# Kernel optimization log

Measured on AMD Instinct MI355X. Metric: run time of the kernel, lower is better.

## Reference

```python
import jax, jax.numpy as jnp
import numpy as np

N_NODES = 50000
HIDDEN = 128
N_EDGES = 800000


def gcn_conv(x, edge_index, W, b):
    # PyG GCNConv: h = x @ W (no bias); add self-loops; symmetric norm; scatter-add; + bias
    h = x @ W  # [N, H]
    row, col = edge_index[0], edge_index[1]
    sl = jnp.arange(N_NODES)
    row_f = jnp.concatenate([row, sl])
    col_f = jnp.concatenate([col, sl])
    ones = jnp.ones(row_f.shape[0], dtype=x.dtype)
    deg = jax.ops.segment_sum(ones, col_f, num_segments=N_NODES)  # in-degree incl self-loop
    dinv = jnp.where(deg > 0, jax.lax.rsqrt(deg), 0.0)
    norm = dinv[row_f] * dinv[col_f]  # [E+N]
    msgs = h[row_f] * norm[:, None]   # gather + scale
    out = jax.ops.segment_sum(msgs, col_f, num_segments=N_NODES)  # scatter-add
    return out + b


def setup_inputs() -> dict:
    key = jax.random.key(0)
    ks = jax.random.split(key, 12)
    H = HIDDEN
    s = 1.0 / np.sqrt(H)
    x = jax.random.normal(ks[0], (N_NODES, H), dtype=jnp.float32)
    edge_index = jax.random.randint(ks[1], (2, N_EDGES), 0, N_NODES, dtype=jnp.int64)
    W1 = jax.random.uniform(ks[2], (H, H), jnp.float32, -s, s)
    b1 = jax.random.uniform(ks[3], (H,), jnp.float32, -s, s)
    W2 = jax.random.uniform(ks[4], (H, H), jnp.float32, -s, s)
    b2 = jax.random.uniform(ks[5], (H,), jnp.float32, -s, s)
    s2 = 1.0 / np.sqrt(2 * H)
    We1 = jax.random.uniform(ks[6], (2 * H, H), jnp.float32, -s2, s2)
    be1 = jax.random.uniform(ks[7], (H,), jnp.float32, -s2, s2)
    We2 = jax.random.uniform(ks[8], (H, 1), jnp.float32, -s, s)
    be2 = jax.random.uniform(ks[9], (1,), jnp.float32, -s, s)
    return {"x": x, "edge_index": edge_index, "W1": W1, "b1": b1, "W2": W2,
            "b2": b2, "We1": We1, "be1": be1, "We2": We2, "be2": be2}


def reference(x, edge_index, W1, b1, W2, b2, We1, be1, We2, be2):
    h = jax.nn.relu(gcn_conv(x, edge_index, W1, b1))
    h = jax.nn.relu(gcn_conv(h, edge_index, W2, b2))
    row, col = edge_index[0], edge_index[1]
    ef = jnp.concatenate([h[row], h[col]], axis=1)  # [E, 2H]
    z = jax.nn.relu(ef @ We1 + be1)
    p = jax.nn.sigmoid(z @ We2 + be2)  # [E, 1]
    return p.squeeze(-1)
```

## Files before the change

### kernel.cpp

```cpp
#include <hip/hip_runtime.h>
#include <math.h>

#define NND 50000
#define HD  128
#define NE  800000
#define NBK 196
#define BINB 391
#define NCH 391

typedef unsigned short u16;
typedef unsigned int   u32;
typedef __attribute__((ext_vector_type(8))) short bf16x8;
typedef __attribute__((ext_vector_type(4))) float f32x4;

__device__ __forceinline__ float bf2f(u32 u) {
  union { u32 i; float f; } v; v.i = u << 16; return v.f;
}
__device__ __forceinline__ u16 f2bf(float f) {
  union { float f; u32 i; } v; v.f = f;
  return (u16)((v.i + 0x7FFFu + ((v.i >> 16) & 1u)) >> 16);
}
__device__ __forceinline__ float4 unpack4(uint2 m) {
  float4 r;
  r.x = bf2f(m.x & 0xFFFFu); r.y = bf2f(m.x >> 16);
  r.z = bf2f(m.y & 0xFFFFu); r.w = bf2f(m.y >> 16);
  return r;
}

__global__ __launch_bounds__(256) void k_hist(const int* __restrict__ col, u32* __restrict__ bhist) {
  __shared__ u32 lh[NBK];
  int tid = threadIdx.x;
  if (tid < NBK) lh[tid] = 0;
  __syncthreads();
  int e0 = blockIdx.x * 2048;
  #pragma unroll
  for (int s = 0; s < 8; ++s) {
    int e = e0 + s * 256 + tid;
    if (e < NE) atomicAdd(&lh[col[e] >> 8], 1u);
  }
  __syncthreads();
  if (tid < NBK && lh[tid]) atomicAdd(&bhist[tid], lh[tid]);
}

__global__ __launch_bounds__(256) void k_bscan(const u32* __restrict__ bhist, u32* __restrict__ bbase,
                                               u32* __restrict__ bcur) {
  __shared__ u32 ws[4];
  int tid = threadIdx.x, lane = tid & 63, wid = tid >> 6;
  u32 d = (tid < NBK) ? bhist[tid] : 0;
  u32 x = d;
  #pragma unroll
  for (int off = 1; off < 64; off <<= 1) {
    u32 y = __shfl_up(x, off);
    if (lane >= off) x += y;
  }
  if (lane == 63) ws[wid] = x;
  __syncthreads();
  u32 woff = 0;
  for (int w = 0; w < wid; ++w) woff += ws[w];
  if (tid < NBK) { bbase[tid] = woff + x - d; bcur[tid] = woff + x - d; }
}

__global__ __launch_bounds__(256) void k_bin(const int* __restrict__ row, const int* __restrict__ col,
                                             u32* __restrict__ bcur, uint2* __restrict__ recs) {
  __shared__ u32 lcount[NBK], lbase[NBK];
  int tid = threadIdx.x;
  if (tid < NBK) lcount[tid] = 0;
  __syncthreads();
  int e0 = blockIdx.x * 2048;
  u32 rank[8]; int cv[8];
  #pragma unroll
  for (int s = 0; s < 8; ++s) {
    int e = e0 + s * 256 + tid;
    if (e < NE) {
      cv[s] = col[e];
      rank[s] = atomicAdd(&lcount[cv[s] >> 8], 1u);
    }
  }
  __syncthreads();
  if (tid < NBK && lcount[tid]) lbase[tid] = atomicAdd(&bcur[tid], lcount[tid]);
  __syncthreads();
  #pragma unroll
  for (int s = 0; s < 8; ++s) {
    int e = e0 + s * 256 + tid;
    if (e < NE) {
      int c = cv[s];
      u32 slot = lbase[c >> 8] + rank[s];
      recs[slot] = make_uint2((u32)row[e] | (((u32)c & 255u) << 16), (u32)e);
    }
  }
}

__global__ __launch_bounds__(256) void k_fine(const u32* __restrict__ bhist, const u32* __restrict__ bbase,
                                              const uint2* __restrict__ recs, uint2* __restrict__ sre,
                                              int* __restrict__ ptr, float* __restrict__ dinv) {
  __shared__ u32 lh[256];
  __shared__ u32 ws[4];
  int b = blockIdx.x, tid = threadIdx.x, lane = tid & 63, wid = tid >> 6;
  u32 base = bbase[b], cnt = bhist[b];
  lh[tid] = 0;
  __syncthreads();
  for (u32 i = tid; i < cnt; i += 256) atomicAdd(&lh[(recs[base + i].x >> 16) & 255u], 1u);
  __syncthreads();
  u32 ci = lh[tid];
  u32 x = ci;
  #pragma unroll
  for (int off = 1; off < 64; off <<= 1) {
    u32 y = __shfl_up(x, off);
    if (lane >= off) x += y;
  }
  if (lane == 63) ws[wid] = x;
  __syncthreads();
  u32 woff = 0;
  for (int w = 0; w < wid; ++w) woff += ws[w];
  u32 excl = woff + x - ci;
  int node = b * 256 + tid;
  if (node <= NND) ptr[node] = (int)(base + excl);
  if (node < NND) dinv[node] = rsqrtf((float)(ci + 1));
  __syncthreads();
  lh[tid] = excl;
  __syncthreads();
  for (u32 i = tid; i < cnt; i += 256) {
    uint2 rec = recs[base + i];
    u32 r = atomicAdd(&lh[(rec.x >> 16) & 255u], 1u);
    sre[base + r] = make_uint2(rec.x & 0xFFFFu, rec.y);
  }
}

__global__ __launch_bounds__(256) void k_wprep(const float* __restrict__ W1, const float* __restrict__ W2,
                                               const float* __restrict__ We1,
                                               u16* __restrict__ t1h, u16* __restrict__ t1l,
                                               u16* __restrict__ t2h, u16* __restrict__ t2l,
                                               u16* __restrict__ teh, u16* __restrict__ tel) {
  int idx = blockIdx.x * 256 + threadIdx.x;
  float w;
  u16 *dh, *dl;
  int j;
  if (idx < 16384) {
    j = idx; int n = j >> 7, k = j & 127;
    w = W1[k * 128 + n]; dh = t1h; dl = t1l;
  } else if (idx < 32768) {
    j = idx - 16384; int n = j >> 7, k = j & 127;
    w = W2[k * 128 + n]; dh = t2h; dl = t2l;
  } else {
    j = idx - 32768; int n = j >> 7, k = j & 127;
    w = (n < 128) ? We1[k * 128 + n] : We1[(128 + k) * 128 + (n - 128)];
    dh = teh; dl = tel;
  }
  int n = j >> 7, k = j & 127;
  int sidx = n * 128 + ((((k >> 3) ^ (n & 7))) << 3) + (k & 7);
  u16 hi = f2bf(w);
  float res = w - bf2f((u32)hi);
  dh[sidx] = hi;
  dl[sidx] = f2bf(res);
}

template<bool AFP32>
__global__ __launch_bounds__(512) void k_mm(const void* __restrict__ Xv,
                                            const u16* __restrict__ Whi, const u16* __restrict__ Wlo,
                                            u16* __restrict__ OUT, const float* __restrict__ scale,
                                            int ostride, int ooff) {
  __shared__ __align__(16) u16 Bh[128 * 128];
  __shared__ __align__(16) u16 Bl[128 * 128];
  int tid = threadIdx.x;
  {
    const uint4* gh = (const uint4*)Whi;
    const uint4* gl = (const uint4*)Wlo;
    uint4* lh = (uint4*)Bh;
    uint4* ll = (uint4*)Bl;
    #pragma unroll
    for (int i = 0; i < 4; ++i) {
      lh[tid + i * 512] = gh[tid + i * 512];
      ll[tid + i * 512] = gl[tid + i * 512];
    }
  }
  __syncthreads();
  int wid = tid >> 6, lane = tid & 63;
  int m16 = lane & 15, kg = lane >> 4;
  for (int chunk = blockIdx.x; chunk < NCH; chunk += gridDim.x) {
    int arow = chunk * 128 + wid * 16 + m16;
    int ar = (arow < NND) ? arow : NND - 1;
    bf16x8 afrag[4];
    if (AFP32) {
      const float* X = (const float*)Xv + (size_t)ar * 128 + kg * 8;
      #pragma unroll
      for (int ks = 0; ks < 4; ++ks) {
        float4 a = *(const float4*)(X + ks * 32);
        float4 b = *(const float4*)(X + ks * 32 + 4);
        union { u32 w[4]; bf16x8 v; } u;
        u.w[0] = (u32)f2bf(a.x) | ((u32)f2bf(a.y) << 16);
        u.w[1] = (u32)f2bf(a.z) | ((u32)f2bf(a.w) << 16);
        u.w[2] = (u32)f2bf(b.x) | ((u32)f2bf(b.y) << 16);
        u.w[3] = (u32)f2bf(b.z) | ((u32)f2bf(b.w) << 16);
        afrag[ks] = u.v;
      }
    } else {
      const u16* X = (const u16*)Xv + (size_t)ar * 128 + kg * 8;
      #pragma unroll
      for (int ks = 0; ks < 4; ++ks) afrag[ks] = *(const bf16x8*)(X + ks * 32);
    }
    int crow0 = chunk * 128 + wid * 16 + kg * 4;
    float sc[4];
    #pragma unroll
    for (int j = 0; j < 4; ++j)
      sc[j] = (scale != nullptr && crow0 + j < NND) ? scale[crow0 + j] : 1.0f;
    #pragma unroll
    for (int t = 0; t < 8; ++t) {
      int coln = t * 16 + m16;
      f32x4 acc = {0.f, 0.f, 0.f, 0.f};
      #pragma unroll
      for (int ks = 0; ks < 4; ++ks) {
        int c8 = (ks * 4 + kg) ^ (coln & 7);
        bf16x8 bhf = *(const bf16x8*)(Bh + coln * 128 + c8 * 8);
        bf16x8 blf = *(const bf16x8*)(Bl + coln * 128 + c8 * 8);
        acc = __builtin_amdgcn_mfma_f32_16x16x32_bf16(afrag[ks], bhf, acc, 0, 0, 0);
        acc = __builtin_amdgcn_mfma_f32_16x16x32_bf16(afrag[ks], blf, acc, 0, 0, 0);
      }
      #pragma unroll
      for (int j = 0; j < 4; ++j) {
        int r = crow0 + j;
        if (r < NND) OUT[(size_t)r * ostride + ooff + coln] = f2bf(acc[j] * sc[j]);
      }
    }
  }
}

__global__ __launch_bounds__(256) void k_gather(const int* __restrict__ ptr, const uint2* __restrict__ sre,
                                                const float* __restrict__ dinv, const u16* __restrict__ Ts,
                                                u16* __restrict__ H, const float* __restrict__ bias) {
  int wid = threadIdx.x >> 6, lane = threadIdx.x & 63;
  int q = lane & 31, eo = lane >> 5;
  int v = blockIdx.x * 4 + wid; if (v >= NND) return;
  int p0 = ptr[v], p1 = ptr[v + 1];
  const uint2* T2 = (const uint2*)Ts;
  float4 acc = make_float4(0.f, 0.f, 0.f, 0.f);
  if (eo == 0) acc = unpack4(T2[(size_t)v * 32 + q]);
  for (int j2 = p0; j2 < p1; j2 += 16) {
    bool ok[8]; int r[8];
    #pragma unroll
    for (int s = 0; s < 8; ++s) {
      int j = j2 + s * 2 + eo;
      ok[s] = j < p1;
      r[s] = (int)sre[ok[s] ? j : p0].x;
    }
    float4 m[8];
    #pragma unroll
    for (int s = 0; s < 8; ++s) m[s] = unpack4(T2[(size_t)r[s] * 32 + q]);
    #pragma unroll
    for (int s = 0; s < 8; ++s)
      if (ok[s]) { acc.x += m[s].x; acc.y += m[s].y; acc.z += m[s].z; acc.w += m[s].w; }
  }
  acc.x += __shfl_xor(acc.x, 32);
  acc.y += __shfl_xor(acc.y, 32);
  acc.z += __shfl_xor(acc.z, 32);
  acc.w += __shfl_xor(acc.w, 32);
  if (eo == 0) {
    float s = dinv[v];
    float4 b = ((const float4*)bias)[q];
    float o0 = fmaxf(fmaf(acc.x, s, b.x), 0.f);
    float o1 = fmaxf(fmaf(acc.y, s, b.y), 0.f);
    float o2 = fmaxf(fmaf(acc.z, s, b.z), 0.f);
    float o3 = fmaxf(fmaf(acc.w, s, b.w), 0.f);
    uint2 o;
    o.x = (u32)f2bf(o0) | ((u32)f2bf(o1) << 16);
    o.y = (u32)f2bf(o2) | ((u32)f2bf(o3) << 16);
    ((uint2*)H)[(size_t)v * 32 + q] = o;
  }
}

__global__ __launch_bounds__(256) void k_edge(const int* __restrict__ ptr, const uint2* __restrict__ sre,
                                              const u16* __restrict__ UV,
                                              const float* __restrict__ be1, const float* __restrict__ We2,
                                              const float* __restrict__ be2, float* __restrict__ out) {
  int wid = threadIdx.x >> 6, lane = threadIdx.x & 63;
  int q = lane & 31, eo = lane >> 5;
  int c = blockIdx.x * 4 + wid; if (c >= NND) return;
  int p0 = ptr[c], p1 = ptr[c + 1];
  if (p0 == p1) return;
  const uint2* UV2 = (const uint2*)UV;
  float4 vv = unpack4(UV2[(size_t)c * 64 + 32 + q]);
  float4 b = ((const float4*)be1)[q];
  vv.x += b.x; vv.y += b.y; vv.z += b.z; vv.w += b.w;
  float4 w2 = ((const float4*)We2)[q];
  float bias2 = be2[0];
  for (int j2 = p0; j2 < p1; j2 += 16) {
    bool ok[8]; uint2 e[8];
    #pragma unroll
    for (int s = 0; s < 8; ++s) {
      int j = j2 + s * 2 + eo;
      ok[s] = j < p1;
      e[s] = sre[ok[s] ? j : p0];
    }
    float4 u[8];
    #pragma unroll
    for (int s = 0; s < 8; ++s) u[s] = unpack4(UV2[(size_t)e[s].x * 64 + q]);
    float p[8];
    #pragma unroll
    for (int s = 0; s < 8; ++s) {
      p[s] = fmaxf(u[s].x + vv.x, 0.f) * w2.x
           + fmaxf(u[s].y + vv.y, 0.f) * w2.y
           + fmaxf(u[s].z + vv.z, 0.f) * w2.z
           + fmaxf(u[s].w + vv.w, 0.f) * w2.w;
    }
    #pragma unroll
    for (int off = 16; off; off >>= 1) {
      #pragma unroll
      for (int s = 0; s < 8; ++s) p[s] += __shfl_xor(p[s], off);
    }
    if (q == 0) {
      #pragma unroll
      for (int s = 0; s < 8; ++s)
        if (ok[s]) out[e[s].y] = 1.f / (1.f + __expf(-(p[s] + bias2)));
    }
  }
}

extern "C" void kernel_launch(void* const* d_in, const int* in_sizes, int n_in,
                              void* d_out, int out_size, void* d_ws, size_t ws_size,
                              hipStream_t stream) {
  const float* x   = (const float*)d_in[0];
  const int*   ei  = (const int*)d_in[1];
  const float* W1  = (const float*)d_in[2];
  const float* b1  = (const float*)d_in[3];
  const float* W2  = (const float*)d_in[4];
  const float* b2  = (const float*)d_in[5];
  const float* We1 = (const float*)d_in[6];
  const float* be1 = (const float*)d_in[7];
  const float* We2 = (const float*)d_in[8];
  const float* be2 = (const float*)d_in[9];
  float* out = (float*)d_out;

  const int* row  = ei;
  const int* colp = ei + NE;

  if (ws_size < (size_t)16166240 * 4) return;
  int*   ptr    = (int*)d_ws;
  float* dinv   = (float*)d_ws + 50064;
  u32*   bhist  = (u32*)d_ws + 100112;
  u32*   bbase  = (u32*)d_ws + 100308;
  u32*   bcur   = (u32*)d_ws + 100504;
  uint2* recs   = (uint2*)((u32*)d_ws + 100704);
  uint2* sre    = (uint2*)((u32*)d_ws + 1700704);
  u16*   t1h    = (u16*)((u32*)d_ws + 3300704);
  u16*   t1l    = (u16*)((u32*)d_ws + 3308896);
  u16*   t2h    = (u16*)((u32*)d_ws + 3317088);
  u16*   t2l    = (u16*)((u32*)d_ws + 3325280);
  u16*   teh    = (u16*)((u32*)d_ws + 3333472);
  u16*   tel    = (u16*)((u32*)d_ws + 3349856);
  u16*   Ts     = (u16*)((u32*)d_ws + 3366240);
  u16*   H      = (u16*)((u32*)d_ws + 6566240);
  u16*   UV     = (u16*)((u32*)d_ws + 9766240);

  hipMemsetAsync(bhist, 0, NBK * sizeof(u32), stream);
  k_wprep<<<256, 256, 0, stream>>>(W1, W2, We1, t1h, t1l, t2h, t2l, teh, tel);
  k_hist <<<BINB, 256, 0, stream>>>(colp, bhist);
  k_bscan<<<1, 256, 0, stream>>>(bhist, bbase, bcur);
  k_bin  <<<BINB, 256, 0, stream>>>(row, colp, bcur, recs);
  k_fine <<<NBK, 256, 0, stream>>>(bhist, bbase, recs, sre, ptr, dinv);

  int node_grid = (NND + 3) / 4;

  k_mm<true><<<196, 512, 0, stream>>>(x, t1h, t1l, Ts, dinv, 128, 0);
  k_gather<<<node_grid, 256, 0, stream>>>(ptr, sre, dinv, Ts, H, b1);

  k_mm<false><<<196, 512, 0, stream>>>(H, t2h, t2l, Ts, dinv, 128, 0);
  k_gather<<<node_grid, 256, 0, stream>>>(ptr, sre, dinv, Ts, H, b2);

  k_mm<false><<<196, 512, 0, stream>>>(H, teh, tel, UV, nullptr, 256, 0);
  k_mm<false><<<196, 512, 0, stream>>>(H, teh + 128 * 128, tel + 128 * 128, UV, nullptr, 256, 128);
  k_edge<<<node_grid, 256, 0, stream>>>(ptr, sre, UV, be1, We2, be2, out);
}
```

Measured before the change: 244.5 us.

## Fuse prep kernels, widen gather/edge loads to 16B, merge edge-matmul launches

Merges the histogram and weight-prep kernels into one launch, and folds the two edge-projection matmuls into a single launch that picks the weight half from the block index. The matmul now uses one block per 128-row chunk instead of a grid-stride loop. The gather and edge kernels switch from 8-byte to 16-byte bf16 loads, with 16 lanes per row and 4 edges in flight per wave, reducing load instructions and shuffle depth. The aim is to cut launch overhead and raise memory-level parallelism on the random gathers, at the cost of reloading the weights into LDS once per chunk block.

Measured after the change: 199.5 us. -18.4%, faster.

```diff
diff --git a/kernel.cpp b/kernel.cpp
--- a/kernel.cpp
+++ b/kernel.cpp
@@ -20,118 +20,35 @@
   union { float f; u32 i; } v; v.f = f;
   return (u16)((v.i + 0x7FFFu + ((v.i >> 16) & 1u)) >> 16);
 }
-__device__ __forceinline__ float4 unpack4(uint2 m) {
-  float4 r;
-  r.x = bf2f(m.x & 0xFFFFu); r.y = bf2f(m.x >> 16);
-  r.z = bf2f(m.y & 0xFFFFu); r.w = bf2f(m.y >> 16);
-  return r;
-}
-
-__global__ __launch_bounds__(256) void k_hist(const int* __restrict__ col, u32* __restrict__ bhist) {
+__device__ __forceinline__ void unpack8(uint4 m, float* f) {
+  f[0] = bf2f(m.x & 0xFFFFu); f[1] = bf2f(m.x >> 16);
+  f[2] = bf2f(m.y & 0xFFFFu); f[3] = bf2f(m.y >> 16);
+  f[4] = bf2f(m.z & 0xFFFFu); f[5] = bf2f(m.z >> 16);
+  f[6] = bf2f(m.w & 0xFFFFu); f[7] = bf2f(m.w >> 16);
+}
+
+__global__ __launch_bounds__(256) void k_prep(const int* __restrict__ col, u32* __restrict__ bhist,
+                                              const float* __restrict__ W1, const float* __restrict__ W2,
+                                              const float* __restrict__ We1,
+                                              u16* __restrict__ t1h, u16* __restrict__ t1l,
+                                              u16* __restrict__ t2h, u16* __restrict__ t2l,
+                                              u16* __restrict__ teh, u16* __restrict__ tel) {
   __shared__ u32 lh[NBK];
   int tid = threadIdx.x;
-  if (tid < NBK) lh[tid] = 0;
-  __syncthreads();
-  int e0 = blockIdx.x * 2048;
-  #pragma unroll
-  for (int s = 0; s < 8; ++s) {
-    int e = e0 + s * 256 + tid;
-    if (e < NE) atomicAdd(&lh[col[e] >> 8], 1u);
-  }
-  __syncthreads();
-  if (tid < NBK && lh[tid]) atomicAdd(&bhist[tid], lh[tid]);
-}
-
-__global__ __launch_bounds__(256) void k_bscan(const u32* __restrict__ bhist, u32* __restrict__ bbase,
-                                               u32* __restrict__ bcur) {
-  __shared__ u32 ws[4];
-  int tid = threadIdx.x, lane = tid & 63, wid = tid >> 6;
-  u32 d = (tid < NBK) ? bhist[tid] : 0;
-  u32 x = d;
-  #pragma unroll
-  for (int off = 1; off < 64; off <<= 1) {
-    u32 y = __shfl_up(x, off);
-    if (lane >= off) x += y;
-  }
-  if (lane == 63) ws[wid] = x;
-  __syncthreads();
-  u32 woff = 0;
-  for (int w = 0; w < wid; ++w) woff += ws[w];
-  if (tid < NBK) { bbase[tid] = woff + x - d; bcur[tid] = woff + x - d; }
-}
-
-__global__ __launch_bounds__(256) void k_bin(const int* __restrict__ row, const int* __restrict__ col,
-                                             u32* __restrict__ bcur, uint2* __restrict__ recs) {
-  __shared__ u32 lcount[NBK], lbase[NBK];
-  int tid = threadIdx.x;
-  if (tid < NBK) lcount[tid] = 0;
-  __syncthreads();
-  int e0 = blockIdx.x * 2048;
-  u32 rank[8]; int cv[8];
-  #pragma unroll
-  for (int s = 0; s < 8; ++s) {
-    int e = e0 + s * 256 + tid;
-    if (e < NE) {
-      cv[s] = col[e];
-      rank[s] = atomicAdd(&lcount[cv[s] >> 8], 1u);
-    }
-  }
-  __syncthreads();
-  if (tid < NBK && lcount[tid]) lbase[tid] = atomicAdd(&bcur[tid], lcount[tid]);
-  __syncthreads();
-  #pragma unroll
-  for (int s = 0; s < 8; ++s) {
-    int e = e0 + s * 256 + tid;
-    if (e < NE) {
-      int c = cv[s];
-      u32 slot = lbase[c >> 8] + rank[s];
-      recs[slot] = make_uint2((u32)row[e] | (((u32)c & 255u) << 16), (u32)e);
-    }
-  }
-}
-
-__global__ __launch_bounds__(256) void k_fine(const u32* __restrict__ bhist, const u32* __restrict__ bbase,
-                                              const uint2* __restrict__ recs, uint2* __restrict__ sre,
-                                              int* __restrict__ ptr, float* __restrict__ dinv) {
-  __shared__ u32 lh[256];
-  __shared__ u32 ws[4];
-  int b = blockIdx.x, tid = threadIdx.x, lane = tid & 63, wid = tid >> 6;
-  u32 base = bbase[b], cnt = bhist[b];
-  lh[tid] = 0;
-  __syncthreads();
-  for (u32 i = tid; i < cnt; i += 256) atomicAdd(&lh[(recs[base + i].x >> 16) & 255u], 1u);
-  __syncthreads();
-  u32 ci = lh[tid];
-  u32 x = ci;
-  #pragma unroll
-  for (int off = 1; off < 64; off <<= 1) {
-    u32 y = __shfl_up(x, off);
-    if (lane >= off) x += y;
-  }
-  if (lane == 63) ws[wid] = x;
-  __syncthreads();
-  u32 woff = 0;
-  for (int w = 0; w < wid; ++w) woff += ws[w];
-  u32 excl = woff + x - ci;
-  int node = b * 256 + tid;
-  if (node <= NND) ptr[node] = (int)(base + excl);
-  if (node < NND) dinv[node] = rsqrtf((float)(ci + 1));
-  __syncthreads();
-  lh[tid] = excl;
-  __syncthreads();
-  for (u32 i = tid; i < cnt; i += 256) {
-    uint2 rec = recs[base + i];
-    u32 r = atomicAdd(&lh[(rec.x >> 16) & 255u], 1u);
-    sre[base + r] = make_uint2(rec.x & 0xFFFFu, rec.y);
-  }
-}
-
-__global__ __launch_bounds__(256) void k_wprep(const float* __restrict__ W1, const float* __restrict__ W2,
-                                               const float* __restrict__ We1,
-                                               u16* __restrict__ t1h, u16* __restrict__ t1l,
-                                               u16* __restrict__ t2h, u16* __restrict__ t2l,
-                                               u16* __restrict__ teh, u16* __restrict__ tel) {
-  int idx = blockIdx.x * 256 + threadIdx.x;
+  if (blockIdx.x < BINB) {
+    if (tid < NBK) lh[tid] = 0;
+    __syncthreads();
+    int e0 = blockIdx.x * 2048;
+    #pragma unroll
+    for (int s = 0; s < 8; ++s) {
+      int e = e0 + s * 256 + tid;
+      if (e < NE) atomicAdd(&lh[col[e] >> 8], 1u);
+    }
+    __syncthreads();
+    if (tid < NBK && lh[tid]) atomicAdd(&bhist[tid], lh[tid]);
+    return;
+  }
+  int idx = (blockIdx.x - BINB) * 256 + tid;
   float w;
   u16 *dh, *dl;
   int j;
@@ -154,14 +71,101 @@
   dl[sidx] = f2bf(res);
 }
 
-template<bool AFP32>
-__global__ __launch_bounds__(512) void k_mm(const void* __restrict__ Xv,
-                                            const u16* __restrict__ Whi, const u16* __restrict__ Wlo,
-                                            u16* __restrict__ OUT, const float* __restrict__ scale,
-                                            int ostride, int ooff) {
+__global__ __launch_bounds__(256) void k_bscan(const u32* __restrict__ bhist, u32* __restrict__ bbase,
+                                               u32* __restrict__ bcur) {
+  __shared__ u32 ws[4];
+  int tid = threadIdx.x, lane = tid & 63, wid = tid >> 6;
+  u32 d = (tid < NBK) ? bhist[tid] : 0;
+  u32 x = d;
+  #pragma unroll
+  for (int off = 1; off < 64; off <<= 1) {
+    u32 y = __shfl_up(x, off);
+    if (lane >= off) x += y;
+  }
+  if (lane == 63) ws[wid] = x;
+  __syncthreads();
+  u32 woff = 0;
+  for (int w = 0; w < wid; ++w) woff += ws[w];
+  if (tid < NBK) { bbase[tid] = woff + x - d; bcur[tid] = woff + x - d; }
+}
+
+__global__ __launch_bounds__(256) void k_bin(const int* __restrict__ row, const int* __restrict__ col,
+                                             u32* __restrict__ bcur, uint2* __restrict__ recs) {
+  __shared__ u32 lcount[NBK], lbase[NBK];
+  int tid = threadIdx.x;
+  if (tid < NBK) lcount[tid] = 0;
+  __syncthreads();
+  int e0 = blockIdx.x * 2048;
+  u32 rank[8]; int cv[8];
+  #pragma unroll
+  for (int s = 0; s < 8; ++s) {
+    int e = e0 + s * 256 + tid;
+    if (e < NE) {
+      cv[s] = col[e];
+      rank[s] = atomicAdd(&lcount[cv[s] >> 8], 1u);
+    }
+  }
+  __syncthreads();
+  if (tid < NBK && lcount[tid]) lbase[tid] = atomicAdd(&bcur[tid], lcount[tid]);
+  __syncthreads();
+  #pragma unroll
+  for (int s = 0; s < 8; ++s) {
+    int e = e0 + s * 256 + tid;
+    if (e < NE) {
+      int c = cv[s];
+      u32 slot = lbase[c >> 8] + rank[s];
+      recs[slot] = make_uint2((u32)row[e] | (((u32)c & 255u) << 16), (u32)e);
+    }
+  }
+}
+
+__global__ __launch_bounds__(256) void k_fine(const u32* __restrict__ bhist, const u32* __restrict__ bbase,
+                                              const uint2* __restrict__ recs, uint2* __restrict__ sre,
+                                              int* __restrict__ ptr, float* __restrict__ dinv) {
+  __shared__ u32 lh[256];
+  __shared__ u32 ws[4];
+  int b = blockIdx.x, tid = threadIdx.x, lane = tid & 63, wid = tid >> 6;
+  u32 base = bbase[b], cnt = bhist[b];
+  lh[tid] = 0;
+  __syncthreads();
+  for (u32 i = tid; i < cnt; i += 256) atomicAdd(&lh[(recs[base + i].x >> 16) & 255u], 1u);
+  __syncthreads();
+  u32 ci = lh[tid];
+  u32 x = ci;
+  #pragma unroll
+  for (int off = 1; off < 64; off <<= 1) {
+    u32 y = __shfl_up(x, off);
+    if (lane >= off) x += y;
+  }
+  if (lane == 63) ws[wid] = x;
+  __syncthreads();
+  u32 woff = 0;
+  for (int w = 0; w < wid; ++w) woff += ws[w];
+  u32 excl = woff + x - ci;
+  int node = b * 256 + tid;
+  if (node <= NND) ptr[node] = (int)(base + excl);
+  if (node < NND) dinv[node] = rsqrtf((float)(ci + 1));
+  __syncthreads();
+  lh[tid] = excl;
+  __syncthreads();
+  for (u32 i = tid; i < cnt; i += 256) {
+    uint2 rec = recs[base + i];
+    u32 r = atomicAdd(&lh[(rec.x >> 16) & 255u], 1u);
+    sre[base + r] = make_uint2(rec.x & 0xFFFFu, rec.y);
+  }
+}
+
+__device__ __forceinline__ void mm_body(const void* Xv, bool afp32,
+                                        const u16* Whi, const u16* Wlo,
+                                        u16* OUT, const float* scale, int ostride) {
   __shared__ __align__(16) u16 Bh[128 * 128];
   __shared__ __align__(16) u16 Bl[128 * 128];
   int tid = threadIdx.x;
+  int h = blockIdx.x / NCH;
+  int chunk = blockIdx.x - h * NCH;
+  Whi += (size_t)h * 128 * 128;
+  Wlo += (size_t)h * 128 * 128;
+  int ooff = h * 128;
   {
     const uint4* gh = (const uint4*)Whi;
     const uint4* gl = (const uint4*)Wlo;
@@ -176,94 +180,114 @@
   __syncthreads();
   int wid = tid >> 6, lane = tid & 63;
   int m16 = lane & 15, kg = lane >> 4;
-  for (int chunk = blockIdx.x; chunk < NCH; chunk += gridDim.x) {
-    int arow = chunk * 128 + wid * 16 + m16;
-    int ar = (arow < NND) ? arow : NND - 1;
-    bf16x8 afrag[4];
-    if (AFP32) {
-      const float* X = (const float*)Xv + (size_t)ar * 128 + kg * 8;
-      #pragma unroll
-      for (int ks = 0; ks < 4; ++ks) {
-        float4 a = *(const float4*)(X + ks * 32);
-        float4 b = *(const float4*)(X + ks * 32 + 4);
-        union { u32 w[4]; bf16x8 v; } u;
-        u.w[0] = (u32)f2bf(a.x) | ((u32)f2bf(a.y) << 16);
-        u.w[1] = (u32)f2bf(a.z) | ((u32)f2bf(a.w) << 16);
-        u.w[2] = (u32)f2bf(b.x) | ((u32)f2bf(b.y) << 16);
-        u.w[3] = (u32)f2bf(b.z) | ((u32)f2bf(b.w) << 16);
-        afrag[ks] = u.v;
-      }
-    } else {
-      const u16* X = (const u16*)Xv + (size_t)ar * 128 + kg * 8;
-      #pragma unroll
-      for (int ks = 0; ks < 4; ++ks) afrag[ks] = *(const bf16x8*)(X + ks * 32);
-    }
-    int crow0 = chunk * 128 + wid * 16 + kg * 4;
-    float sc[4];
-    #pragma unroll
-    for (int j = 0; j < 4; ++j)
-      sc[j] = (scale != nullptr && crow0 + j < NND) ? scale[crow0 + j] : 1.0f;
-    #pragma unroll
-    for (int t = 0; t < 8; ++t) {
-      int coln = t * 16 + m16;
-      f32x4 acc = {0.f, 0.f, 0.f, 0.f};
-      #pragma unroll
-      for (int ks = 0; ks < 4; ++ks) {
-        int c8 = (ks * 4 + kg) ^ (coln & 7);
-        bf16x8 bhf = *(const bf16x8*)(Bh + coln * 128 + c8 * 8);
-        bf16x8 blf = *(const bf16x8*)(Bl + coln * 128 + c8 * 8);
-        acc = __builtin_amdgcn_mfma_f32_16x16x32_bf16(afrag[ks], bhf, acc, 0, 0, 0);
-        acc = __builtin_amdgcn_mfma_f32_16x16x32_bf16(afrag[ks], blf, acc, 0, 0, 0);
-      }
-      #pragma unroll
-      for (int j = 0; j < 4; ++j) {
-        int r = crow0 + j;
-        if (r < NND) OUT[(size_t)r * ostride + ooff + coln] = f2bf(acc[j] * sc[j]);
-      }
-    }
-  }
+  int arow = chunk * 128 + wid * 16 + m16;
+  int ar = (arow < NND) ? arow : NND - 1;
+  bf16x8 afrag[4];
+  if (afp32) {
+    const float* X = (const float*)Xv + (size_t)ar * 128 + kg * 8;
+    #pragma unroll
+    for (int ks = 0; ks < 4; ++ks) {
+      float4 a = *(const float4*)(X + ks * 32);
+      float4 b = *(const float4*)(X + ks * 32 + 4);
+      union { u32 w[4]; bf16x8 v; } u;
+      u.w[0] = (u32)f2bf(a.x) | ((u32)f2bf(a.y) << 16);
+      u.w[1] = (u32)f2bf(a.z) | ((u32)f2bf(a.w) << 16);
+      u.w[2] = (u32)f2bf(b.x) | ((u32)f2bf(b.y) << 16);
+      u.w[3] = (u32)f2bf(b.z) | ((u32)f2bf(b.w) << 16);
+      afrag[ks] = u.v;
+    }
+  } else {
+    const u16* X = (const u16*)Xv + (size_t)ar * 128 + kg * 8;
+    #pragma unroll
+    for (int ks = 0; ks < 4; ++ks) afrag[ks] = *(const bf16x8*)(X + ks * 32);
+  }
+  int crow0 = chunk * 128 + wid * 16 + kg * 4;
+  float sc[4];
+  #pragma unroll
+  for (int j = 0; j < 4; ++j)
+    sc[j] = (scale != nullptr && crow0 + j < NND) ? scale[crow0 + j] : 1.0f;
+  #pragma unroll
+  for (int t = 0; t < 8; ++t) {
+    int coln = t * 16 + m16;
+    f32x4 acc = {0.f, 0.f, 0.f, 0.f};
+    #pragma unroll
+    for (int ks = 0; ks < 4; ++ks) {
+      int c8 = (ks * 4 + kg) ^ (coln & 7);
+      bf16x8 bhf = *(const bf16x8*)(Bh + coln * 128 + c8 * 8);
+      bf16x8 blf = *(const bf16x8*)(Bl + coln * 128 + c8 * 8);
+      acc = __builtin_amdgcn_mfma_f32_16x16x32_bf16(afrag[ks], bhf, acc, 0, 0, 0);
+      acc = __builtin_amdgcn_mfma_f32_16x16x32_bf16(afrag[ks], blf, acc, 0, 0, 0);
+    }
+    #pragma unroll
+    for (int j = 0; j < 4; ++j) {
+      int r = crow0 + j;
+      if (r < NND) OUT[(size_t)r * ostride + ooff + coln] = f2bf(acc[j] * sc[j]);
+    }
+  }
+}
+
+template<bool AFP32>
+__global__ __launch_bounds__(512) void k_mm(const void* __restrict__ Xv,
+                                            const u16* __restrict__ Whi, const u16* __restrict__ Wlo,
+                                            u16* __restrict__ OUT, const float* __restrict__ scale,
+                                            int ostride) {
+  mm_body(Xv, AFP32, Whi, Wlo, OUT, scale, ostride);
 }
 
 __global__ __launch_bounds__(256) void k_gather(const int* __restrict__ ptr, const uint2* __restrict__ sre,
                                                 const float* __restrict__ dinv, const u16* __restrict__ Ts,
                                                 u16* __restrict__ H, const float* __restrict__ bias) {
   int wid = threadIdx.x >> 6, lane = threadIdx.x & 63;
-  int q = lane & 31, eo = lane >> 5;
+  int ch8 = lane & 15, slot = lane >> 4;
   int v = blockIdx.x * 4 + wid; if (v >= NND) return;
   int p0 = ptr[v], p1 = ptr[v + 1];
-  const uint2* T2 = (const uint2*)Ts;
-  float4 acc = make_float4(0.f, 0.f, 0.f, 0.f);
-  if (eo == 0) acc = unpack4(T2[(size_t)v * 32 + q]);
-  for (int j2 = p0; j2 < p1; j2 += 16) {
+  const uint4* T4 = (const uint4*)Ts;
+  float acc[8];
+  if (slot == 0) {
+    uint4 m = T4[(size_t)v * 16 + ch8];
+    unpack8(m, acc);
+  } else {
+    #pragma unroll
+    for (int k = 0; k < 8; ++k) acc[k] = 0.f;
+  }
+  for (int j2 = p0; j2 < p1; j2 += 32) {
     bool ok[8]; int r[8];
     #pragma unroll
-    for (int s = 0; s < 8; ++s) {
-      int j = j2 + s * 2 + eo;
-      ok[s] = j < p1;
-      r[s] = (int)sre[ok[s] ? j : p0].x;
-    }
-    float4 m[8];
-    #pragma unroll
-    for (int s = 0; s < 8; ++s) m[s] = unpack4(T2[(size_t)r[s] * 32 + q]);
-    #pragma unroll
-    for (int s = 0; s < 8; ++s)
-      if (ok[s]) { acc.x += m[s].x; acc.y += m[s].y; acc.z += m[s].z; acc.w += m[s].w; }
-  }
-  acc.x += __shfl_xor(acc.x, 32);
-  acc.y += __shfl_xor(acc.y, 32);
-  acc.z += __shfl_xor(acc.z, 32);
-  acc.w += __shfl_xor(acc.w, 32);
-  if (eo == 0) {
+    for (int u = 0; u < 8; ++u) {
+      int j = j2 + u * 4 + slot;
+      ok[u] = j < p1;
+      r[u] = (int)sre[ok[u] ? j : p0].x;
+    }
+    uint4 m[8];
+    #pragma unroll
+    for (int u = 0; u < 8; ++u) m[u] = T4[(size_t)r[u] * 16 + ch8];
+    #pragma unroll
+    for (int u = 0; u < 8; ++u) {
+      if (ok[u]) {
+        float f[8]; unpack8(m[u], f);
+        #pragma unroll
+        for (int k = 0; k < 8; ++k) acc[k] += f[k];
+      }
+    }
+  }
+  #pragma unroll
+  for (int k = 0; k < 8; ++k) {
+    acc[k] += __shfl_xor(acc[k], 16);
+    acc[k] += __shfl_xor(acc[k], 32);
+  }
+  if (slot == 0) {
     float s = dinv[v];
-    float4 b = ((const float4*)bias)[q];
-    float o0 = fmaxf(fmaf(acc.x, s, b.x), 0.f);
-    float o1 = fmaxf(fmaf(acc.y, s, b.y), 0.f);
-    float o2 = fmaxf(fmaf(acc.z, s, b.z), 0.f);
-    float o3 = fmaxf(fmaf(acc.w, s, b.w), 0.f);
-    uint2 o;
-    o.x = (u32)f2bf(o0) | ((u32)f2bf(o1) << 16);
-    o.y = (u32)f2bf(o2) | ((u32)f2bf(o3) << 16);
-    ((uint2*)H)[(size_t)v * 32 + q] = o;
+    float4 ba = *(const float4*)(bias + ch8 * 8);
+    float4 bb = *(const float4*)(bias + ch8 * 8 + 4);
+    float bv[8] = {ba.x, ba.y, ba.z, ba.w, bb.x, bb.y, bb.z, bb.w};
+    u32 pk[4];
+    #pragma unroll
+    for (int k = 0; k < 4; ++k) {
+      float o0 = fmaxf(fmaf(acc[2 * k], s, bv[2 * k]), 0.f);
+      float o1 = fmaxf(fmaf(acc[2 * k + 1], s, bv[2 * k + 1]), 0.f);
+      pk[k] = (u32)f2bf(o0) | ((u32)f2bf(o1) << 16);
+    }
+    *(uint4*)(H + (size_t)v * 128 + ch8 * 8) = make_uint4(pk[0], pk[1], pk[2], pk[3]);
   }
 }
 
@@ -272,44 +296,58 @@
                                               const float* __restrict__ be1, const float* __restrict__ We2,
                                               const float* __restrict__ be2, float* __restrict__ out) {
   int wid = threadIdx.x >> 6, lane = threadIdx.x & 63;
-  int q = lane & 31, eo = lane >> 5;
+  int ch8 = lane & 15, slot = lane >> 4;
   int c = blockIdx.x * 4 + wid; if (c >= NND) return;
   int p0 = ptr[c], p1 = ptr[c + 1];
   if (p0 == p1) return;
-  const uint2* UV2 = (const uint2*)UV;
-  float4 vv = unpack4(UV2[(size_t)c * 64 + 32 + q]);
-  float4 b = ((const float4*)be1)[q];
-  vv.x += b.x; vv.y += b.y; vv.z += b.z; vv.w += b.w;
-  float4 w2 = ((const float4*)We2)[q];
+  const uint4* UV4 = (const uint4*)UV;
+  float vv[8];
+  {
+    uint4 mv = UV4[(size_t)c * 32 + 16 + ch8];
+    unpack8(mv, vv);
+    float4 ba = *(const float4*)(be1 + ch8 * 8);
+    float4 bb = *(const float4*)(be1 + ch8 * 8 + 4);
+    vv[0] += ba.x; vv[1] += ba.y; vv[2] += ba.z; vv[3] += ba.w;
+    vv[4] += bb.x; vv[5] += bb.y; vv[6] += bb.z; vv[7] += bb.w;
+  }
+  float w2[8];
+  {
+    float4 wa = *(const float4*)(We2 + ch8 * 8);
+    float4 wb = *(const float4*)(We2 + ch8 * 8 + 4);
+    w2[0] = wa.x; w2[1] = wa.y; w2[2] = wa.z; w2[3] = wa.w;
+    w2[4] = wb.x; w2[5] = wb.y; w2[6] = wb.z; w2[7] = wb.w;
+  }
   float bias2 = be2[0];
-  for (int j2 = p0; j2 < p1; j2 += 16) {
+  for (int j2 = p0; j2 < p1; j2 += 32) {
     bool ok[8]; uint2 e[8];
     #pragma unroll
-    for (int s = 0; s < 8; ++s) {
-      int j = j2 + s * 2 + eo;
-      ok[s] = j < p1;
-      e[s] = sre[ok[s] ? j : p0];
-    }
-    float4 u[8];
-    #pragma unroll
-    for (int s = 0; s < 8; ++s) u[s] = unpack4(UV2[(size_t)e[s].x * 64 + q]);
+    for (int u = 0; u < 8; ++u) {
+      int j = j2 + u * 4 + slot;
+      ok[u] = j < p1;
+      e[u] = sre[ok[u] ? j : p0];
+    }
+    uint4 m[8];
+    #pragma unroll
+    for (int u = 0; u < 8; ++u) m[u] = UV4[(size_t)e[u].x * 32 + ch8];
     float p[8];
     #pragma unroll
-    for (int s = 0; s < 8; ++s) {
-      p[s] = fmaxf(u[s].x + vv.x, 0.f) * w2.x
-           + fmaxf(u[s].y + vv.y, 0.f) * w2.y
-           + fmaxf(u[s].z + vv.z, 0.f) * w2.z
-           + fmaxf(u[s].w + vv.w, 0.f) * w2.w;
-    }
-    #pragma unroll
-    for (int off = 16; off; off >>= 1) {
+    for (int u = 0; u < 8; ++u) {
+      float f[8]; unpack8(m[u], f);
+      float s0 = fmaxf(f[0] + vv[0], 0.f) * w2[0] + fmaxf(f[1] + vv[1], 0.f) * w2[1];
+      s0 += fmaxf(f[2] + vv[2], 0.f) * w2[2] + fmaxf(f[3] + vv[3], 0.f) * w2[3];
+      s0 += fmaxf(f[4] + vv[4], 0.f) * w2[4] + fmaxf(f[5] + vv[5], 0.f) * w2[5];
+      s0 += fmaxf(f[6] + vv[6], 0.f) * w2[6] + fmaxf(f[7] + vv[7], 0.f) * w2[7];
+      p[u] = s0;
+    }
+    #pragma unroll
+    for (int off = 8; off; off >>= 1) {
       #pragma unroll
-      for (int s = 0; s < 8; ++s) p[s] += __shfl_xor(p[s], off);
-    }
-    if (q == 0) {
+      for (int u = 0; u < 8; ++u) p[u] += __shfl_xor(p[u], off);
+    }
+    if (ch8 == 0) {
       #pragma unroll
-      for (int s = 0; s < 8; ++s)
-        if (ok[s]) out[e[s].y] = 1.f / (1.f + __expf(-(p[s] + bias2)));
+      for (int u = 0; u < 8; ++u)
+        if (ok[u]) out[e[u].y] = 1.f / (1.f + __expf(-(p[u] + bias2)));
     }
   }
 }
@@ -350,22 +388,20 @@
   u16*   H      = (u16*)((u32*)d_ws + 6566240);
   u16*   UV     = (u16*)((u32*)d_ws + 9766240);
 
-  hipMemsetAsync(bhist, 0, NBK * sizeof(u32), stream);
-  k_wprep<<<256, 256, 0, stream>>>(W1, W2, We1, t1h, t1l, t2h, t2l, teh, tel);
-  k_hist <<<BINB, 256, 0, stream>>>(colp, bhist);
+  (void)hipMemsetAsync(bhist, 0, NBK * sizeof(u32), stream);
+  k_prep <<<BINB + 256, 256, 0, stream>>>(colp, bhist, W1, W2, We1, t1h, t1l, t2h, t2l, teh, tel);
   k_bscan<<<1, 256, 0, stream>>>(bhist, bbase, bcur);
   k_bin  <<<BINB, 256, 0, stream>>>(row, colp, bcur, recs);
   k_fine <<<NBK, 256, 0, stream>>>(bhist, bbase, recs, sre, ptr, dinv);
 
   int node_grid = (NND + 3) / 4;
 
-  k_mm<true><<<196, 512, 0, stream>>>(x, t1h, t1l, Ts, dinv, 128, 0);
+  k_mm<true><<<NCH, 512, 0, stream>>>(x, t1h, t1l, Ts, dinv, 128);
   k_gather<<<node_grid, 256, 0, stream>>>(ptr, sre, dinv, Ts, H, b1);
 
-  k_mm<false><<<196, 512, 0, stream>>>(H, t2h, t2l, Ts, dinv, 128, 0);
+  k_mm<false><<<NCH, 512, 0, stream>>>(H, t2h, t2l, Ts, dinv, 128);
   k_gather<<<node_grid, 256, 0, stream>>>(ptr, sre, dinv, Ts, H, b2);
 
-  k_mm<false><<<196, 512, 0, stream>>>(H, teh, tel, UV, nullptr, 256, 0);
-  k_mm<false><<<196, 512, 0, stream>>>(H, teh + 128 * 128, tel + 128 * 128, UV, nullptr, 256, 128);
+  k_mm<false><<<2 * NCH, 512, 0, stream>>>(H, teh, tel, UV, nullptr, 256);
   k_edge<<<node_grid, 256, 0, stream>>>(ptr, sre, UV, be1, We2, be2, out);
 }
```
